# Kernel optimization log

Hardware: AMD Instinct MI355X
Metric: run time of the kernel (lower is better)

The kernel has to match this reference:

```python
import jax, jax.numpy as jnp
import numpy as np

N_NODES = 100000
N_EDGES = 1600000


def setup_inputs() -> dict:
    key = jax.random.key(0)
    ks = jax.random.split(key, 12)
    inp = {
        "x": jax.random.normal(ks[0], (N_NODES, 8), dtype=jnp.float32),
        "edge_index": jax.random.randint(ks[1], (2, N_EDGES), 0, N_NODES, dtype=jnp.int32),
        "W1_l": jax.random.normal(ks[2], (8, 64), dtype=jnp.float32) * 0.1,
        "b1": jax.random.normal(ks[3], (64,), dtype=jnp.float32) * 0.1,
        "W1_r": jax.random.normal(ks[4], (8, 64), dtype=jnp.float32) * 0.1,
        "W2_l": jax.random.normal(ks[5], (64, 64), dtype=jnp.float32) * 0.1,
        "b2": jax.random.normal(ks[6], (64,), dtype=jnp.float32) * 0.1,
        "W2_r": jax.random.normal(ks[7], (64, 64), dtype=jnp.float32) * 0.1,
        "fc1_W": jax.random.normal(ks[8], (64, 64), dtype=jnp.float32) * 0.1,
        "fc1_b": jax.random.normal(ks[9], (64,), dtype=jnp.float32) * 0.1,
        "fc2_W": jax.random.normal(ks[10], (64, 10), dtype=jnp.float32) * 0.1,
        "fc2_b": jax.random.normal(ks[11], (10,), dtype=jnp.float32) * 0.1,
    }
    return inp


def _sage_conv(x, edge_index, W_l, b_l, W_r, num_nodes):
    """PyG SAGEConv (mean aggr): lin_l(mean_j x_j) + lin_r(x_i)."""
    src, dst = edge_index[0], edge_index[1]
    msg = x[src]  # (E, F) gather
    summed = jax.ops.segment_sum(msg, dst, num_segments=num_nodes)  # (N, F)
    deg = jax.ops.segment_sum(jnp.ones((edge_index.shape[1],), dtype=x.dtype), dst,
                              num_segments=num_nodes)
    mean = summed / jnp.maximum(deg, 1.0)[:, None]
    return mean @ W_l + b_l + x @ W_r


def reference(x, edge_index, W1_l, b1, W1_r, W2_l, b2, W2_r, fc1_W, fc1_b, fc2_W, fc2_b):
    n = x.shape[0]
    h = jax.nn.relu(_sage_conv(x, edge_index, W1_l, b1, W1_r, n))
    h = jax.nn.relu(_sage_conv(h, edge_index, W2_l, b2, W2_r, n))
    # global_mean_pool with all-zero batch ids == mean over all nodes -> (1, 64)
    g = jnp.mean(h, axis=0, keepdims=True)
    a = jax.nn.relu(g @ fc1_W + fc1_b)
    a = a @ fc2_W + fc2_b
    return jax.nn.softmax(a, axis=-1)
```

## Files before the change

kernel.cpp:

```cpp
#include <hip/hip_runtime.h>
#include <hip/hip_bf16.h>
#include <hip/hip_fp16.h>

#define N_NODES 100000
#define N_EDGES 1600000
#define NBUCK ((N_NODES + 255) >> 8)
#define CAP 8192
#define NMT (N_NODES / 16)
#define SBLK 512
#define SCHUNK ((N_EDGES + SBLK - 1) / SBLK)

typedef _Float16 f16x8 __attribute__((ext_vector_type(8)));
typedef float f32x4 __attribute__((ext_vector_type(4)));

__device__ inline float2 h2_to_f2(unsigned int u) {
    __half2 h = *reinterpret_cast<__half2*>(&u);
    return __half22float2(h);
}

__global__ void k_zero(int* __restrict__ p, int n) {
    for (int i = threadIdx.x; i < n; i += 256) p[i] = 0;
}

__global__ __launch_bounds__(512) void k_stage(const int* __restrict__ src,
                                               const int* __restrict__ dst,
                                               int* __restrict__ bcursor,
                                               unsigned int* __restrict__ stage) {
    __shared__ int h[512];
    __shared__ int loc[512];
    __shared__ int base[NBUCK];
    __shared__ int cur[NBUCK];
    __shared__ unsigned int buf[SCHUNK];
    __shared__ int gidx[SCHUNK];
    const int tid = threadIdx.x;
    const int c0 = blockIdx.x * SCHUNK;
    const int c1 = (c0 + SCHUNK < N_EDGES) ? (c0 + SCHUNK) : N_EDGES;

    h[tid] = 0;
    if (tid < NBUCK) cur[tid] = 0;
    __syncthreads();

    for (int e = c0 + tid; e < c1; e += 512)
        atomicAdd(&h[dst[e] >> 8], 1);
    __syncthreads();

    int v = h[tid];
    loc[tid] = v;
    __syncthreads();
    for (int d = 1; d < 512; d <<= 1) {
        int t = (tid >= d) ? loc[tid - d] : 0;
        __syncthreads();
        loc[tid] += t;
        __syncthreads();
    }
    int inc = loc[tid];
    __syncthreads();
    loc[tid] = inc - v;
    if (tid < NBUCK && v > 0) base[tid] = atomicAdd(&bcursor[tid], v);
    __syncthreads();

    for (int e = c0 + tid; e < c1; e += 512) {
        int d = dst[e];
        int b = d >> 8;
        int pos = loc[b] + atomicAdd(&cur[b], 1);
        buf[pos] = ((unsigned int)(d & 255) << 17) | (unsigned int)src[e];
        int gpos = base[b] + (pos - loc[b]);
        gidx[pos] = (gpos < CAP) ? (b * CAP + gpos) : -1;
    }
    __syncthreads();

    const int cnt = c1 - c0;
    for (int i = tid; i < cnt; i += 512) {
        int g = gidx[i];
        if (g >= 0) stage[g] = buf[i];
    }
}

__global__ __launch_bounds__(512) void k_bsort(unsigned int* __restrict__ stage,
                                               const int* __restrict__ bcursor,
                                               int* __restrict__ row_start,
                                               int* __restrict__ deg) {
    __shared__ int off[256];
    __shared__ int cur[256];
    __shared__ unsigned int out[CAP];
    const int b = blockIdx.x;
    int cnt = bcursor[b];
    if (cnt > CAP) cnt = CAP;
    const int s = b * CAP;
    const int tid = threadIdx.x;

    if (tid < 256) cur[tid] = 0;
    __syncthreads();
    for (int i = tid; i < cnt; i += 512)
        atomicAdd(&cur[stage[s + i] >> 17], 1);
    __syncthreads();
    int v = 0;
    if (tid < 256) {
        v = cur[tid];
        off[tid] = v;
    }
    __syncthreads();
    for (int d = 1; d < 256; d <<= 1) {
        int t = 0;
        if (tid < 256 && tid >= d) t = off[tid - d];
        __syncthreads();
        if (tid < 256) off[tid] += t;
        __syncthreads();
    }
    if (tid < 256) {
        int ex = off[tid] - v;
        off[tid] = ex;
        cur[tid] = 0;
        int node = b * 256 + tid;
        if (node < N_NODES) {
            row_start[node] = s + ex;
            deg[node] = v;
        }
    }
    __syncthreads();

    for (int i = tid; i < cnt; i += 512) {
        unsigned int p = stage[s + i];
        int l = p >> 17;
        int pos = off[l] + atomicAdd(&cur[l], 1);
        out[pos] = p & 0x1FFFFu;
    }
    __syncthreads();
    for (int i = tid; i < cnt; i += 512)
        stage[s + i] = out[i];
}

__global__ __launch_bounds__(256) void layer1(
    const float* __restrict__ x, const int* __restrict__ row_start,
    const int* __restrict__ deg, const int* __restrict__ csr,
    const float* __restrict__ W1l, const float* __restrict__ b1,
    const float* __restrict__ W1r, __half* __restrict__ h1h) {
    const int lane = threadIdx.x & 63;
    const int g = lane >> 3;
    const int sub = lane & 7;

    float wl1[8], wr1[8];
#pragma unroll
    for (int k = 0; k < 8; k++) {
        wl1[k] = W1l[k * 64 + lane];
        wr1[k] = W1r[k * 64 + lane];
    }
    float bv = b1[lane];
    asm volatile("" ::: "memory");

    const int gwid = (blockIdx.x * blockDim.x + threadIdx.x) >> 6;
    const int nwaves = (gridDim.x * blockDim.x) >> 6;

    for (int node = gwid; node < N_NODES; node += nwaves) {
        int rs = row_start[node];
        int dg = deg[node];
        int re = rs + dg;
        float acc = 0.0f;
        int t = rs;
        for (; t + 16 <= re; t += 16) {
            int i0 = csr[t + g];
            int i1 = csr[t + 8 + g];
            acc += x[i0 * 8 + sub] + x[i1 * 8 + sub];
        }
        for (; t + 8 <= re; t += 8) {
            int i0 = csr[t + g];
            acc += x[i0 * 8 + sub];
        }
        int r = re - t;
        if (r > 0) {
            int ii = csr[(t + g < re) ? (t + g) : (re - 1)];
            float v = x[ii * 8 + sub];
            if (g < r) acc += v;
        }
        acc += __shfl_xor(acc, 8);
        acc += __shfl_xor(acc, 16);
        acc += __shfl_xor(acc, 32);
        float inv = 1.0f / fmaxf((float)dg, 1.0f);
        float mean = acc * inv;
        float xself = x[node * 8 + sub];
        float m[8], xk[8];
#pragma unroll
        for (int k = 0; k < 8; k++) {
            m[k]  = __shfl(mean, k);
            xk[k] = __shfl(xself, k);
        }
        float a = bv;
#pragma unroll
        for (int k = 0; k < 8; k++)
            a += m[k] * wl1[k] + xk[k] * wr1[k];
        h1h[node * 64 + lane] = __float2half(fmaxf(a, 0.0f));
    }
}

__global__ __launch_bounds__(256) void agg2(
    const __half* __restrict__ h1h, const int* __restrict__ row_start,
    const int* __restrict__ deg, const int* __restrict__ csr,
    __half* __restrict__ mean2h) {
    const int lane = threadIdx.x & 63;
    const int g = lane >> 4;
    const int sub = lane & 15;

    const int gwid = (blockIdx.x * blockDim.x + threadIdx.x) >> 6;
    const int nwaves = (gridDim.x * blockDim.x) >> 6;

    for (int node = gwid; node < N_NODES; node += nwaves) {
        int rs = row_start[node];
        int dg = deg[node];
        int re = rs + dg;
        float4 acc = {0.f, 0.f, 0.f, 0.f};
        int t = rs;
        for (; t + 8 <= re; t += 8) {
            int i0 = csr[t + g];
            int i1 = csr[t + 4 + g];
            uint2 a = *(const uint2*)(h1h + i0 * 64 + sub * 4);
            uint2 b = *(const uint2*)(h1h + i1 * 64 + sub * 4);
            float2 a0 = h2_to_f2(a.x), a1 = h2_to_f2(a.y);
            float2 b0 = h2_to_f2(b.x), b1 = h2_to_f2(b.y);
            acc.x += a0.x + b0.x; acc.y += a0.y + b0.y;
            acc.z += a1.x + b1.x; acc.w += a1.y + b1.y;
        }
        for (; t + 4 <= re; t += 4) {
            int i0 = csr[t + g];
            uint2 a = *(const uint2*)(h1h + i0 * 64 + sub * 4);
            float2 a0 = h2_to_f2(a.x), a1 = h2_to_f2(a.y);
            acc.x += a0.x; acc.y += a0.y; acc.z += a1.x; acc.w += a1.y;
        }
        int r = re - t;
        if (r > 0) {
            int ii = csr[(t + g < re) ? (t + g) : (re - 1)];
            uint2 a = *(const uint2*)(h1h + ii * 64 + sub * 4);
            if (g < r) {
                float2 a0 = h2_to_f2(a.x), a1 = h2_to_f2(a.y);
                acc.x += a0.x; acc.y += a0.y; acc.z += a1.x; acc.w += a1.y;
            }
        }
#pragma unroll
        for (int m = 16; m <= 32; m <<= 1) {
            acc.x += __shfl_xor(acc.x, m);
            acc.y += __shfl_xor(acc.y, m);
            acc.z += __shfl_xor(acc.z, m);
            acc.w += __shfl_xor(acc.w, m);
        }
        float inv = 1.0f / fmaxf((float)dg, 1.0f);
        if (lane < 16) {
            __half2 o0 = __floats2half2_rn(acc.x * inv, acc.y * inv);
            __half2 o1 = __floats2half2_rn(acc.z * inv, acc.w * inv);
            uint2 pk;
            pk.x = *(unsigned int*)&o0;
            pk.y = *(unsigned int*)&o1;
            *(uint2*)(mean2h + node * 64 + sub * 4) = pk;
        }
    }
}

__global__ __launch_bounds__(256) void mlp2_mfma(
    const __half* __restrict__ mean2h, const __half* __restrict__ h1h,
    const float* __restrict__ W2l, const float* __restrict__ b2,
    const float* __restrict__ W2r, float* __restrict__ gsum) {
    __shared__ float part[4][64];
    const int tid = threadIdx.x;
    const int lane = tid & 63;
    const int w = tid >> 6;
    const int row16 = lane & 15;
    const int grp = lane >> 4;

    f16x8 bf[4][4];
#pragma unroll
    for (int c = 0; c < 4; c++) {
        const float* Wsrc = (c < 2) ? W2l : W2r;
        int koff = (c & 1) * 32 + grp * 8;
#pragma unroll
        for (int nt = 0; nt < 4; nt++) {
            f16x8 t;
#pragma unroll
            for (int j = 0; j < 8; j++)
                t[j] = (_Float16)Wsrc[(koff + j) * 64 + nt * 16 + row16];
            bf[c][nt] = t;
        }
    }
    float bv[4];
#pragma unroll
    for (int nt = 0; nt < 4; nt++) bv[nt] = b2[nt * 16 + row16];
    asm volatile("" ::: "memory");

    const int gwid = (blockIdx.x * blockDim.x + tid) >> 6;
    const int nwaves = (gridDim.x * blockDim.x) >> 6;
    float pool[4] = {0.f, 0.f, 0.f, 0.f};

    for (int mt = gwid; mt < NMT; mt += nwaves) {
        int n0 = mt * 16;
        const __half* am = mean2h + (size_t)(n0 + row16) * 64 + grp * 8;
        const __half* ah = h1h    + (size_t)(n0 + row16) * 64 + grp * 8;
        f16x8 af[4];
        af[0] = *(const f16x8*)(am);
        af[1] = *(const f16x8*)(am + 32);
        af[2] = *(const f16x8*)(ah);
        af[3] = *(const f16x8*)(ah + 32);
#pragma unroll
        for (int nt = 0; nt < 4; nt++) {
            f32x4 acc = {bv[nt], bv[nt], bv[nt], bv[nt]};
#pragma unroll
            for (int c = 0; c < 4; c++)
                acc = __builtin_amdgcn_mfma_f32_16x16x32_f16(af[c], bf[c][nt],
                                                             acc, 0, 0, 0);
            pool[nt] += fmaxf(acc[0], 0.f) + fmaxf(acc[1], 0.f) +
                        fmaxf(acc[2], 0.f) + fmaxf(acc[3], 0.f);
        }
    }

#pragma unroll
    for (int nt = 0; nt < 4; nt++) {
        pool[nt] += __shfl_xor(pool[nt], 16);
        pool[nt] += __shfl_xor(pool[nt], 32);
    }
    if (lane < 16) {
#pragma unroll
        for (int nt = 0; nt < 4; nt++)
            part[w][nt * 16 + row16] = pool[nt];
    }
    __syncthreads();
    if (tid < 64)
        atomicAdd(&gsum[tid],
                  part[0][tid] + part[1][tid] + part[2][tid] + part[3][tid]);
}

__global__ void head(const float* __restrict__ gsum,
                     const float* __restrict__ fc1W, const float* __restrict__ fc1b,
                     const float* __restrict__ fc2W, const float* __restrict__ fc2b,
                     float* __restrict__ out) {
    __shared__ float g[64];
    __shared__ float a1[64];
    __shared__ float a2[10];
    int j = threadIdx.x;
    g[j] = gsum[j] * (1.0f / (float)N_NODES);
    __syncthreads();
    float acc = fc1b[j];
    for (int k = 0; k < 64; k++) acc += g[k] * fc1W[k * 64 + j];
    a1[j] = fmaxf(acc, 0.0f);
    __syncthreads();
    if (j < 10) {
        float acc2 = fc2b[j];
        for (int k = 0; k < 64; k++) acc2 += a1[k] * fc2W[k * 10 + j];
        a2[j] = acc2;
    }
    __syncthreads();
    if (j == 0) {
        float mx = -1e30f;
        for (int i = 0; i < 10; i++) mx = fmaxf(mx, a2[i]);
        float s = 0.0f;
        float e[10];
        for (int i = 0; i < 10; i++) {
            e[i] = expf(a2[i] - mx);
            s += e[i];
        }
        float invs = 1.0f / s;
        for (int i = 0; i < 10; i++) out[i] = e[i] * invs;
    }
}

extern "C" void kernel_launch(void* const* d_in, const int* in_sizes, int n_in,
                              void* d_out, int out_size, void* d_ws, size_t ws_size,
                              hipStream_t stream) {
    const float* x    = (const float*)d_in[0];
    const int*   ei   = (const int*)d_in[1];
    const float* W1l  = (const float*)d_in[2];
    const float* b1   = (const float*)d_in[3];
    const float* W1r  = (const float*)d_in[4];
    const float* W2l  = (const float*)d_in[5];
    const float* b2   = (const float*)d_in[6];
    const float* W2r  = (const float*)d_in[7];
    const float* fc1W = (const float*)d_in[8];
    const float* fc1b = (const float*)d_in[9];
    const float* fc2W = (const float*)d_in[10];
    const float* fc2b = (const float*)d_in[11];
    float* out = (float*)d_out;

    const int* src = ei;
    const int* dst = ei + N_EDGES;

    __half* h1h    = (__half*)d_ws;
    unsigned int* stage = (unsigned int*)(h1h + (size_t)N_NODES * 64);
    int* csr       = (int*)stage;
    __half* mean2h = (__half*)(stage + (size_t)NBUCK * CAP);
    int* row_start = (int*)(mean2h + (size_t)N_NODES * 64);
    int* deg       = row_start + N_NODES;
    int* bcursor   = deg + N_NODES;
    float* gsum    = (float*)(bcursor + NBUCK);

    k_zero<<<1, 256, 0, stream>>>(bcursor, NBUCK + 64);

    k_stage<<<SBLK, 512, 0, stream>>>(src, dst, bcursor, stage);
    k_bsort<<<NBUCK, 512, 0, stream>>>(stage, bcursor, row_start, deg);
    layer1<<<2048, 256, 0, stream>>>(x, row_start, deg, csr, W1l, b1, W1r, h1h);
    agg2<<<2048, 256, 0, stream>>>(h1h, row_start, deg, csr, mean2h);
    mlp2_mfma<<<512, 256, 0, stream>>>(mean2h, h1h, W2l, b2, W2r, gsum);
    head<<<1, 64, 0, stream>>>(gsum, fc1W, fc1b, fc2W, fc2b, out);
}
```

Baseline: 126.4 us.

## Fuse layer-1 aggregation into bucket sort kernel using shared-memory CSR

```diff
diff --git a/kernel.cpp b/kernel.cpp
--- a/kernel.cpp
+++ b/kernel.cpp
@@ -76,11 +76,13 @@
     }
 }
 
-__global__ __launch_bounds__(512) void k_bsort(unsigned int* __restrict__ stage,
-                                               const int* __restrict__ bcursor,
-                                               int* __restrict__ row_start,
-                                               int* __restrict__ deg) {
-    __shared__ int off[256];
+__global__ __launch_bounds__(512) void k_bsort_l1(
+    unsigned int* __restrict__ stage, const int* __restrict__ bcursor,
+    int* __restrict__ row_start, int* __restrict__ deg,
+    const float* __restrict__ x, const float* __restrict__ W1l,
+    const float* __restrict__ b1, const float* __restrict__ W1r,
+    __half* __restrict__ h1h) {
+    __shared__ int off[257];
     __shared__ int cur[256];
     __shared__ unsigned int out[CAP];
     const int b = blockIdx.x;
@@ -116,6 +118,7 @@
             row_start[node] = s + ex;
             deg[node] = v;
         }
+        if (tid == 255) off[256] = cnt;
     }
     __syncthreads();
 
@@ -128,14 +131,10 @@
     __syncthreads();
     for (int i = tid; i < cnt; i += 512)
         stage[s + i] = out[i];
-}
-
-__global__ __launch_bounds__(256) void layer1(
-    const float* __restrict__ x, const int* __restrict__ row_start,
-    const int* __restrict__ deg, const int* __restrict__ csr,
-    const float* __restrict__ W1l, const float* __restrict__ b1,
-    const float* __restrict__ W1r, __half* __restrict__ h1h) {
-    const int lane = threadIdx.x & 63;
+
+    __syncthreads();
+    const int lane = tid & 63;
+    const int w = tid >> 6;
     const int g = lane >> 3;
     const int sub = lane & 7;
 
@@ -146,31 +145,29 @@
         wr1[k] = W1r[k * 64 + lane];
     }
     float bv = b1[lane];
-    asm volatile("" ::: "memory");
-
-    const int gwid = (blockIdx.x * blockDim.x + threadIdx.x) >> 6;
-    const int nwaves = (gridDim.x * blockDim.x) >> 6;
-
-    for (int node = gwid; node < N_NODES; node += nwaves) {
-        int rs = row_start[node];
-        int dg = deg[node];
-        int re = rs + dg;
+
+    for (int local = w * 32; local < w * 32 + 32; ++local) {
+        int node = b * 256 + local;
+        if (node >= N_NODES) break;
+        int rs = off[local];
+        int re = off[local + 1];
+        int dg = re - rs;
         float acc = 0.0f;
         int t = rs;
         for (; t + 16 <= re; t += 16) {
-            int i0 = csr[t + g];
-            int i1 = csr[t + 8 + g];
+            int i0 = (int)out[t + g];
+            int i1 = (int)out[t + 8 + g];
             acc += x[i0 * 8 + sub] + x[i1 * 8 + sub];
         }
         for (; t + 8 <= re; t += 8) {
-            int i0 = csr[t + g];
+            int i0 = (int)out[t + g];
             acc += x[i0 * 8 + sub];
         }
         int r = re - t;
         if (r > 0) {
-            int ii = csr[(t + g < re) ? (t + g) : (re - 1)];
-            float v = x[ii * 8 + sub];
-            if (g < r) acc += v;
+            int ii = (int)out[(t + g < re) ? (t + g) : (re - 1)];
+            float vv = x[ii * 8 + sub];
+            if (g < r) acc += vv;
         }
         acc += __shfl_xor(acc, 8);
         acc += __shfl_xor(acc, 16);
@@ -188,7 +185,7 @@
 #pragma unroll
         for (int k = 0; k < 8; k++)
             a += m[k] * wl1[k] + xk[k] * wr1[k];
-        h1h[node * 64 + lane] = __float2half(fmaxf(a, 0.0f));
+        h1h[(size_t)node * 64 + lane] = __float2half(fmaxf(a, 0.0f));
     }
 }
 
@@ -390,8 +387,8 @@
     k_zero<<<1, 256, 0, stream>>>(bcursor, NBUCK + 64);
 
     k_stage<<<SBLK, 512, 0, stream>>>(src, dst, bcursor, stage);
-    k_bsort<<<NBUCK, 512, 0, stream>>>(stage, bcursor, row_start, deg);
-    layer1<<<2048, 256, 0, stream>>>(x, row_start, deg, csr, W1l, b1, W1r, h1h);
+    k_bsort_l1<<<NBUCK, 512, 0, stream>>>(stage, bcursor, row_start, deg,
+                                          x, W1l, b1, W1r, h1h);
     agg2<<<2048, 256, 0, stream>>>(h1h, row_start, deg, csr, mean2h);
     mlp2_mfma<<<512, 256, 0, stream>>>(mean2h, h1h, W2l, b2, W2r, gsum);
     head<<<1, 64, 0, stream>>>(gsum, fc1W, fc1b, fc2W, fc2b, out);
```

New measurement: 135.1 us. 6.8% more time.
